# Performance work log

Hardware: AMD Instinct MI355X
Metric: run time of the kernel (lower is better)

Reference implementation:

```python
import jax, jax.numpy as jnp
import numpy as np

N_NODES = 100000


def gcn_conv(x, src, dst, W, b, n):
    # PyG GCNConv: add self-loops, symmetric deg^-1/2 normalization,
    # linear transform, gather->scatter-add aggregation, + bias.
    loop = jnp.arange(n, dtype=src.dtype)
    s = jnp.concatenate([src, loop])
    d = jnp.concatenate([dst, loop])
    deg = jax.ops.segment_sum(jnp.ones_like(d, dtype=x.dtype), d, num_segments=n)
    dinv = jnp.where(deg > 0, jax.lax.rsqrt(deg), jnp.zeros_like(deg))
    norm = dinv[s] * dinv[d]            # [E+N]
    h = x @ W                            # [N, out] (transform before propagate)
    msg = h[s] * norm[:, None]           # gather + scale
    out = jax.ops.segment_sum(msg, d, num_segments=n)  # scatter-add to dst
    return out + b


def setup_inputs() -> dict:
    key = jax.random.key(0)
    k = jax.random.split(key, 6)
    n, e, c_in, hid, c_out = N_NODES, 2500000, 5, 32, 1
    x = jax.random.normal(k[0], (n, c_in), dtype=jnp.float32)
    edge_index = jax.random.randint(k[1], (2, e), 0, n, dtype=jnp.int64)
    # Glorot-style init for GCN weights, zero bias (PyG default)
    W1 = jax.random.normal(k[2], (c_in, hid), dtype=jnp.float32) * (1.0 / np.sqrt(c_in))
    b1 = jnp.zeros((hid,), dtype=jnp.float32)
    W2 = jax.random.normal(k[3], (hid, c_out), dtype=jnp.float32) * (1.0 / np.sqrt(hid))
    b2 = jnp.zeros((c_out,), dtype=jnp.float32)
    return {"x": x, "edge_index": edge_index, "W1": W1, "b1": b1, "W2": W2, "b2": b2}


def reference(x, edge_index, W1, b1, W2, b2):
    n = x.shape[0]
    src, dst = edge_index[0], edge_index[1]
    h = jax.nn.relu(gcn_conv(x, src, dst, W1, b1, n))
    # dropout p=0.3 is identity at inference (training=False)
    return jax.nn.sigmoid(gcn_conv(h, src, dst, W2, b2, n))
```

## Files before the change

### kernel.cpp

```cpp
#include <hip/hip_runtime.h>
#include <math.h>


#define NB_SHIFT  8
#define BNODES    256
#define NBK       512
#define CAP       8192
#define CAP_SHIFT 13
#define CHUNK     4888
#define PBLK      512

__global__ void k_init(int* __restrict__ bcur) {
    int b = threadIdx.x;
    if (b < NBK) bcur[b] = b << CAP_SHIFT;
}

__global__ __launch_bounds__(PBLK) void k_part(const int* __restrict__ src,
                                               const int* __restrict__ dst, int E,
                                               int* __restrict__ bcur,
                                               int* __restrict__ pairs) {
    __shared__ int sp[CHUNK];
    __shared__ unsigned short sb[CHUNK];
    __shared__ int cnt[NBK], ofs[NBK], cur[NBK], gbase[NBK];
    int tid = threadIdx.x;
    int base = blockIdx.x * CHUNK;
    int m = min(CHUNK, E - base);

    if (tid < NBK) cnt[tid] = 0;
    __syncthreads();
    for (int i = tid; i < m; i += PBLK)
        atomicAdd(&cnt[dst[base + i] >> NB_SHIFT], 1);
    __syncthreads();
    int v = cnt[tid];
    ofs[tid] = v;
    __syncthreads();
    for (int off = 1; off < NBK; off <<= 1) {
        int u = (tid >= off) ? ofs[tid - off] : 0;
        __syncthreads();
        ofs[tid] += u;
        __syncthreads();
    }
    int pre = ofs[tid] - v;
    ofs[tid] = pre;
    cur[tid] = pre;
    gbase[tid] = v ? atomicAdd(&bcur[tid], v) : 0;
    __syncthreads();
    for (int i = tid; i < m; i += PBLK) {
        int s = src[base + i], d = dst[base + i];
        int b = d >> NB_SHIFT;
        int p = atomicAdd(&cur[b], 1);
        sp[p] = ((d & (BNODES - 1)) << 24) | s;
        sb[p] = (unsigned short)b;
    }
    __syncthreads();
    for (int i = tid; i < m; i += PBLK) {
        int b = sb[i];
        pairs[gbase[b] + (i - ofs[b])] = sp[i];
    }
}

__global__ __launch_bounds__(512) void k_sorta(const int* __restrict__ pairs,
                                               const int* __restrict__ bcur,
                                               const float* __restrict__ x,
                                               float* __restrict__ dinv,
                                               float* __restrict__ xs,
                                               int* __restrict__ nofs,
                                               int* __restrict__ deg, int n) {
    __shared__ int cnt[BNODES], scn[BNODES];
    int tid = threadIdx.x;
    int b = blockIdx.x;
    int base = b << CAP_SHIFT;
    int len = min(bcur[b] - base, CAP);

    if (tid < BNODES) cnt[tid] = 0;
    __syncthreads();
    for (int i = tid; i < len; i += 512)
        atomicAdd(&cnt[((unsigned)pairs[base + i]) >> 24], 1);
    __syncthreads();
    int v = (tid < BNODES) ? cnt[tid] : 0;
    if (tid < BNODES) scn[tid] = v;
    __syncthreads();
    for (int off = 1; off < BNODES; off <<= 1) {
        int u = (tid < BNODES && tid >= off) ? scn[tid - off] : 0;
        __syncthreads();
        if (tid < BNODES) scn[tid] += u;
        __syncthreads();
    }
    if (tid < BNODES) {
        int node = (b << NB_SHIFT) + tid;
        if (node < n) {
            nofs[node] = base + scn[tid] - v;
            deg[node] = v;
            float di = rsqrtf((float)v + 1.0f);
            dinv[node] = di;
            const float* xr = x + (size_t)node * 5;
            float* xo = xs + ((size_t)node << 3);
#pragma unroll
            for (int k = 0; k < 5; ++k) xo[k] = xr[k] * di;
        }
    }
}

__global__ __launch_bounds__(512) void k_sortagg1(int* __restrict__ pairs,
                                                  const int* __restrict__ bcur,
                                                  const int* __restrict__ nofs,
                                                  const int* __restrict__ deg,
                                                  const float* __restrict__ xs,
                                                  const float* __restrict__ dinv,
                                                  const float* __restrict__ W1,
                                                  const float* __restrict__ b1,
                                                  const float* __restrict__ W2,
                                                  float* __restrict__ h2s, int n) {
    __shared__ int stage2[CAP];
    __shared__ int ofs[BNODES], cnt[BNODES], cur[BNODES];
    __shared__ float w1[160], bb1[32], w2[32];
    int tid = threadIdx.x;
    int b = blockIdx.x;
    int nbase = b << NB_SHIFT;
    int base = b << CAP_SHIFT;
    int len = min(bcur[b] - base, CAP);

    if (tid < 160) w1[tid] = W1[tid];
    else if (tid < 192) bb1[tid - 160] = b1[tid - 160];
    else if (tid < 224) w2[tid - 192] = W2[tid - 192];
    if (tid < BNODES) {
        int node = nbase + tid;
        int o = 0, c = 0;
        if (node < n) { o = nofs[node] - base; c = deg[node]; }
        ofs[tid] = o; cnt[tid] = c; cur[tid] = o;
    }
    __syncthreads();
    for (int i = tid; i < len; i += 512) {
        int vv = pairs[base + i];
        int p = atomicAdd(&cur[((unsigned)vv) >> 24], 1);
        stage2[p] = vv & 0x00FFFFFF;
    }
    __syncthreads();
    for (int i = tid; i < len; i += 512) pairs[base + i] = stage2[i];
    int t2 = tid >> 1, half = tid & 1;
    int node = nbase + t2;
    if (node >= n) return;
    int beg = ofs[t2], dg = cnt[t2];
    float a0 = 0.f, a1 = 0.f, a2 = 0.f, a3 = 0.f, a4 = 0.f;
    if (!half) {
        const float* xo = xs + ((size_t)node << 3);
        a0 = xo[0]; a1 = xo[1]; a2 = xo[2]; a3 = xo[3]; a4 = xo[4];
    }
    for (int e = beg + half; e < beg + dg; e += 2) {
        int s = stage2[e];
        const float* xr = xs + ((size_t)s << 3);
        float4 q = *(const float4*)xr;
        float q4 = xr[4];
        a0 += q.x; a1 += q.y; a2 += q.z; a3 += q.w; a4 += q4;
    }
    a0 += __shfl_xor(a0, 1); a1 += __shfl_xor(a1, 1); a2 += __shfl_xor(a2, 1);
    a3 += __shfl_xor(a3, 1); a4 += __shfl_xor(a4, 1);
    if (half) return;
    float di = dinv[node];
    a0 *= di; a1 *= di; a2 *= di; a3 *= di; a4 *= di;
    float sum = 0.f;
#pragma unroll
    for (int c = 0; c < 32; ++c) {
        float z = bb1[c] + a0 * w1[c] + a1 * w1[32 + c] + a2 * w1[64 + c]
                         + a3 * w1[96 + c] + a4 * w1[128 + c];
        sum += fmaxf(z, 0.f) * w2[c];
    }
    h2s[node] = sum * di;
}

__global__ __launch_bounds__(256) void k_agg2(const int* __restrict__ pairs,
                                              const int* __restrict__ nofs,
                                              const int* __restrict__ deg,
                                              const float* __restrict__ h2s,
                                              const float* __restrict__ dinv,
                                              const float* __restrict__ b2,
                                              float* __restrict__ out, int n) {
    int tid = threadIdx.x;
    int node = blockIdx.x * 128 + (tid >> 1);
    int half = tid & 1;
    if (node >= n) return;
    int beg = nofs[node], dg = deg[node];
    float a = 0.f;
    for (int e = beg + half; e < beg + dg; e += 2) a += h2s[pairs[e]];
    a += __shfl_xor(a, 1);
    if (half) return;
    float v = dinv[node] * (a + h2s[node]) + b2[0];
    out[node] = 1.0f / (1.0f + __expf(-v));
}

extern "C" void kernel_launch(void* const* d_in, const int* in_sizes, int n_in,
                              void* d_out, int out_size, void* d_ws, size_t ws_size,
                              hipStream_t stream) {
    const float* x  = (const float*)d_in[0];
    const int*   ei = (const int*)d_in[1];
    const float* W1 = (const float*)d_in[2];
    const float* b1 = (const float*)d_in[3];
    const float* W2 = (const float*)d_in[4];
    const float* b2 = (const float*)d_in[5];
    float* out = (float*)d_out;

    const int n = in_sizes[0] / 5;
    const int E = in_sizes[1] / 2;
    const int* src = ei;
    const int* dst = ei + E;
    const int nb = (n + BNODES - 1) >> NB_SHIFT;

    int* wsi = (int*)d_ws;
    int*   pairs = wsi;
    int*   nofs  = wsi + ((size_t)(nb + 1) << CAP_SHIFT);
    int*   deg   = nofs + n;
    float* dinv  = (float*)(deg + n);
    float* h2s   = dinv + n;
    float* xs    = h2s + n;
    int*   bcur  = (int*)(xs + (size_t)8 * n);

    const int nchunk = (E + CHUNK - 1) / CHUNK;
    const int nagg   = (n + 127) / 128;

    k_init<<<1, NBK, 0, stream>>>(bcur);
    k_part<<<nchunk, PBLK, 0, stream>>>(src, dst, E, bcur, pairs);
    k_sorta<<<nb, 512, 0, stream>>>(pairs, bcur, x, dinv, xs, nofs, deg, n);
    k_sortagg1<<<nb, 512, 0, stream>>>(pairs, bcur, nofs, deg, xs, dinv,
                                       W1, b1, W2, h2s, n);
    k_agg2<<<nagg, 256, 0, stream>>>(pairs, nofs, deg, h2s, dinv, b2, out, n);
}
```

Before: 146.5 us.

## Unroll partition loops by two, widen agg2 to 4 lanes, memset bucket counters

Replaces the init kernel with a memset and makes bucket counters relative offsets. The partition and first sort loops are manually unrolled by two so each thread issues two independent loads before its shared atomics. The second aggregation now uses four lanes per node instead of two, which exposes more memory-level parallelism on the gathers. The cost is more lanes sitting idle on low-degree nodes and a memset call that may or may not be cheaper than the tiny kernel it replaces.

```diff
diff --git a/kernel.cpp b/kernel.cpp
--- a/kernel.cpp
+++ b/kernel.cpp
@@ -10,11 +10,6 @@
 #define CHUNK     4888
 #define PBLK      512
 
-__global__ void k_init(int* __restrict__ bcur) {
-    int b = threadIdx.x;
-    if (b < NBK) bcur[b] = b << CAP_SHIFT;
-}
-
 __global__ __launch_bounds__(PBLK) void k_part(const int* __restrict__ src,
                                                const int* __restrict__ dst, int E,
                                                int* __restrict__ bcur,
@@ -28,8 +23,13 @@
 
     if (tid < NBK) cnt[tid] = 0;
     __syncthreads();
-    for (int i = tid; i < m; i += PBLK)
-        atomicAdd(&cnt[dst[base + i] >> NB_SHIFT], 1);
+    for (int i = tid; i < m; i += 2 * PBLK) {
+        int i1 = i + PBLK;
+        int k0 = dst[base + i] >> NB_SHIFT;
+        int k1 = (i1 < m) ? (dst[base + i1] >> NB_SHIFT) : -1;
+        atomicAdd(&cnt[k0], 1);
+        if (k1 >= 0) atomicAdd(&cnt[k1], 1);
+    }
     __syncthreads();
     int v = cnt[tid];
     ofs[tid] = v;
@@ -43,14 +43,23 @@
     int pre = ofs[tid] - v;
     ofs[tid] = pre;
     cur[tid] = pre;
-    gbase[tid] = v ? atomicAdd(&bcur[tid], v) : 0;
-    __syncthreads();
-    for (int i = tid; i < m; i += PBLK) {
-        int s = src[base + i], d = dst[base + i];
-        int b = d >> NB_SHIFT;
-        int p = atomicAdd(&cur[b], 1);
-        sp[p] = ((d & (BNODES - 1)) << 24) | s;
-        sb[p] = (unsigned short)b;
+    gbase[tid] = (tid << CAP_SHIFT) + (v ? atomicAdd(&bcur[tid], v) : 0);
+    __syncthreads();
+    for (int i = tid; i < m; i += 2 * PBLK) {
+        int i1 = i + PBLK;
+        int s0 = src[base + i], d0 = dst[base + i];
+        int s1 = 0, d1 = 0;
+        if (i1 < m) { s1 = src[base + i1]; d1 = dst[base + i1]; }
+        int b0 = d0 >> NB_SHIFT;
+        int p0 = atomicAdd(&cur[b0], 1);
+        sp[p0] = ((d0 & (BNODES - 1)) << 24) | s0;
+        sb[p0] = (unsigned short)b0;
+        if (i1 < m) {
+            int b1 = d1 >> NB_SHIFT;
+            int p1 = atomicAdd(&cur[b1], 1);
+            sp[p1] = ((d1 & (BNODES - 1)) << 24) | s1;
+            sb[p1] = (unsigned short)b1;
+        }
     }
     __syncthreads();
     for (int i = tid; i < m; i += PBLK) {
@@ -70,7 +79,7 @@
     int tid = threadIdx.x;
     int b = blockIdx.x;
     int base = b << CAP_SHIFT;
-    int len = min(bcur[b] - base, CAP);
+    int len = min(bcur[b], CAP);
 
     if (tid < BNODES) cnt[tid] = 0;
     __syncthreads();
@@ -118,7 +127,7 @@
     int b = blockIdx.x;
     int nbase = b << NB_SHIFT;
     int base = b << CAP_SHIFT;
-    int len = min(bcur[b] - base, CAP);
+    int len = min(bcur[b], CAP);
 
     if (tid < 160) w1[tid] = W1[tid];
     else if (tid < 192) bb1[tid - 160] = b1[tid - 160];
@@ -130,10 +139,16 @@
         ofs[tid] = o; cnt[tid] = c; cur[tid] = o;
     }
     __syncthreads();
-    for (int i = tid; i < len; i += 512) {
-        int vv = pairs[base + i];
-        int p = atomicAdd(&cur[((unsigned)vv) >> 24], 1);
-        stage2[p] = vv & 0x00FFFFFF;
+    for (int i = tid; i < len; i += 1024) {
+        int i1 = i + 512;
+        int v0 = pairs[base + i];
+        int v1 = (i1 < len) ? pairs[base + i1] : -1;
+        int p0 = atomicAdd(&cur[((unsigned)v0) >> 24], 1);
+        stage2[p0] = v0 & 0x00FFFFFF;
+        if (v1 != -1) {
+            int p1 = atomicAdd(&cur[((unsigned)v1) >> 24], 1);
+            stage2[p1] = v1 & 0x00FFFFFF;
+        }
     }
     __syncthreads();
     for (int i = tid; i < len; i += 512) pairs[base + i] = stage2[i];
@@ -176,14 +191,15 @@
                                               const float* __restrict__ b2,
                                               float* __restrict__ out, int n) {
     int tid = threadIdx.x;
-    int node = blockIdx.x * 128 + (tid >> 1);
-    int half = tid & 1;
+    int node = blockIdx.x * 64 + (tid >> 2);
+    int q = tid & 3;
     if (node >= n) return;
     int beg = nofs[node], dg = deg[node];
     float a = 0.f;
-    for (int e = beg + half; e < beg + dg; e += 2) a += h2s[pairs[e]];
+    for (int e = beg + q; e < beg + dg; e += 4) a += h2s[pairs[e]];
     a += __shfl_xor(a, 1);
-    if (half) return;
+    a += __shfl_xor(a, 2);
+    if (q) return;
     float v = dinv[node] * (a + h2s[node]) + b2[0];
     out[node] = 1.0f / (1.0f + __expf(-v));
 }
@@ -215,9 +231,9 @@
     int*   bcur  = (int*)(xs + (size_t)8 * n);
 
     const int nchunk = (E + CHUNK - 1) / CHUNK;
-    const int nagg   = (n + 127) / 128;
-
-    k_init<<<1, NBK, 0, stream>>>(bcur);
+    const int nagg   = (n + 63) / 64;
+
+    hipMemsetAsync(bcur, 0, NBK * sizeof(int), stream);
     k_part<<<nchunk, PBLK, 0, stream>>>(src, dst, E, bcur, pairs);
     k_sorta<<<nb, 512, 0, stream>>>(pairs, bcur, x, dinv, xs, nofs, deg, n);
     k_sortagg1<<<nb, 512, 0, stream>>>(pairs, bcur, nofs, deg, xs, dinv,
```

Result: no change. 144.6 us (-1.3%).
